# Kernel optimization log

Hardware: AMD Instinct MI355X
Metric: run time of the kernel (lower is better)

Reference implementation:

```python
import jax, jax.numpy as jnp
import numpy as np

N = 50000
E = 800000
F_IN = 64
F_OUT = 64


def setup_inputs() -> dict:
    key = jax.random.key(0)
    k1, k2, k3, k4, k5, k6 = jax.random.split(key, 6)
    x = jax.random.normal(k1, (N, F_IN), dtype=jnp.float32)
    x0 = jax.random.normal(k2, (N, F_IN), dtype=jnp.float32)
    edge_index = jax.random.randint(k3, (2, E), 0, N, dtype=jnp.int64)
    # Linear(in_channels, out_channels): weight [out, in], bias [out]
    bound = 1.0 / np.sqrt(F_IN)
    W_w = jax.random.uniform(k4, (F_OUT, F_IN), minval=-bound, maxval=bound, dtype=jnp.float32)
    W_b = jax.random.uniform(k5, (F_OUT,), minval=-bound, maxval=bound, dtype=jnp.float32)
    return {"x": x, "x0": x0, "edge_index": edge_index, "W_w": W_w, "W_b": W_b}


def reference(x, x0, edge_index, W_w, W_b):
    row, col = edge_index[0], edge_index[1]
    n = x.shape[0]
    # degree of each node as a destination (counts of col)
    d = jax.ops.segment_sum(jnp.ones_like(col, dtype=jnp.float32), col, num_segments=n)
    # per-edge symmetric normalization 1/sqrt(d[col]*d[row]); nan_to_num -> 0 where degree 0
    d_in = d[col]
    d_out = d[row]
    value = jnp.where((d_in > 0) & (d_out > 0),
                      jax.lax.rsqrt(jnp.maximum(d_in, 1.0)) * jax.lax.rsqrt(jnp.maximum(d_out, 1.0)),
                      0.0)
    # SpMM: adj has (row=col, col=row) so out[col_e] += value_e * x[row_e]
    msg = value[:, None] * x[row]                     # [E, F]
    agg = jax.ops.segment_sum(msg, col, num_segments=n)  # [N, F]
    # use_init=False, use_weight=True -> dense Linear
    return agg @ W_w.T + W_b
```

## Files before the change

### kernel.cpp

```cpp
#include <hip/hip_runtime.h>

#define NN 50000
#define NE 800000
#define FDIM 64
#define NB 8
#define P1B 768
#define RCAP 256
#define CAP 64
#define OVFCAP 16384
#define NPX 6250
#define GEMMB ((NN + 63) / 64)
#define E4 (NE / 4)
#define CHUNK4 ((E4 + P1B - 1) / P1B)

typedef float f32x4 __attribute__((ext_vector_type(4)));

__device__ __forceinline__ unsigned rne_bf16(float f) {
    unsigned u = __float_as_uint(f);
    return (u + 0x7fffu + ((u >> 16) & 1u)) >> 16;
}

__global__ __launch_bounds__(256) void k_part(
        const int4* __restrict__ row4, const int4* __restrict__ col4,
        unsigned* __restrict__ buckets, int* __restrict__ bcnt,
        int* __restrict__ cnt, unsigned* __restrict__ ovf, int* __restrict__ ovfcnt) {
    int gid = blockIdx.x * 256 + threadIdx.x;
    for (int i = gid; i < NN; i += P1B * 256) cnt[i] = 0;
    if (gid == 0) *ovfcnt = 0;

    __shared__ int lcnt[NB];
    if (threadIdx.x < NB) lcnt[threadIdx.x] = 0;
    __syncthreads();

    int start = blockIdx.x * CHUNK4;
    int end   = min(start + CHUNK4, E4);
    for (int i = start + (int)threadIdx.x; i < end; i += 256) {
        int4 r4 = row4[i];
        int4 c4 = col4[i];
        int rr[4] = {r4.x, r4.y, r4.z, r4.w};
        int cc[4] = {c4.x, c4.y, c4.z, c4.w};
#pragma unroll
        for (int t = 0; t < 4; ++t) {
            int c = cc[t];
            int b = (int)(((unsigned long long)(unsigned)c * 687195ull) >> 32);
            unsigned pk = ((unsigned)rr[t] << 16) | (unsigned)c;
            int slot = atomicAdd(&lcnt[b], 1);
            if (slot < RCAP)
                buckets[(size_t)(b * P1B + blockIdx.x) * RCAP + slot] = pk;
            else {
                int o = atomicAdd(ovfcnt, 1);
                if (o >= 0 && o < OVFCAP) ovf[o] = pk;
            }
        }
    }
    __syncthreads();
    if (threadIdx.x < NB)
        bcnt[threadIdx.x * P1B + blockIdx.x] = min(lcnt[threadIdx.x], RCAP);
}

__global__ __launch_bounds__(256) void k_gemm(const float* __restrict__ x,
                                              const float* __restrict__ W,
                                              unsigned* __restrict__ z) {
    __shared__ float Xl[64][68];
    __shared__ float Wt[64][68];

    for (int i = threadIdx.x; i < FDIM * FDIM; i += 256) {
        int o = i >> 6, k = i & 63;
        Wt[k][o] = W[i];
    }
    int tile = blockIdx.x * 64;
    for (int i = threadIdx.x; i < 64 * 16; i += 256) {
        int r = i >> 4, c4 = i & 15;
        int gr = tile + r;
        f32x4 v = (gr < NN) ? ((const f32x4*)x)[gr * 16 + c4]
                            : (f32x4){0.f, 0.f, 0.f, 0.f};
        *(f32x4*)&Xl[r][c4 * 4] = v;
    }
    __syncthreads();

    int tr = threadIdx.x >> 4;
    int tc = threadIdx.x & 15;

    float acc[4][4] = {};
#pragma unroll 1
    for (int k4 = 0; k4 < 16; ++k4) {
        f32x4 a[4], b[4];
#pragma unroll
        for (int i = 0; i < 4; ++i)
            a[i] = *(const f32x4*)&Xl[tr * 4 + i][k4 * 4];
#pragma unroll
        for (int kk = 0; kk < 4; ++kk)
            b[kk] = *(const f32x4*)&Wt[k4 * 4 + kk][tc * 4];
#pragma unroll
        for (int i = 0; i < 4; ++i) {
#pragma unroll
            for (int jj = 0; jj < 4; ++jj) {
                acc[i][jj] += a[i].x * b[0][jj] + a[i].y * b[1][jj]
                            + a[i].z * b[2][jj] + a[i].w * b[3][jj];
            }
        }
    }

#pragma unroll
    for (int i = 0; i < 4; ++i) {
        int gr = tile + tr * 4 + i;
        if (gr < NN) {
            unsigned u01 = rne_bf16(acc[i][0]) | (rne_bf16(acc[i][1]) << 16);
            unsigned u23 = rne_bf16(acc[i][2]) | (rne_bf16(acc[i][3]) << 16);
            ((uint2*)z)[gr * 16 + tc] = make_uint2(u01, u23);
        }
    }
}

__global__ __launch_bounds__(256) void k_fill(const unsigned* __restrict__ buckets,
                                              const int* __restrict__ bcnt,
                                              int* __restrict__ cnt,
                                              unsigned short* __restrict__ erow,
                                              unsigned* __restrict__ ovf,
                                              int* __restrict__ ovfcnt) {
    int k  = blockIdx.x & (NB - 1);
    int b1 = blockIdx.x >> 3;
    int m  = bcnt[k * P1B + b1];
    const unsigned* reg = buckets + (size_t)(k * P1B + b1) * RCAP;
    for (int i = threadIdx.x; i < m; i += 256) {
        unsigned pk = reg[i];
        int c = (int)(pk & 0xffffu), r = (int)(pk >> 16);
        int p = atomicAdd(&cnt[c], 1);
        if (p < CAP) erow[c * CAP + p] = (unsigned short)r;
        else {
            int o = atomicAdd(ovfcnt, 1);
            if (o >= 0 && o < OVFCAP) ovf[o] = pk;
        }
    }
}

__global__ __launch_bounds__(256) void k_gather(
        const int* __restrict__ cnt, const unsigned short* __restrict__ erow,
        const uint4* __restrict__ z4, const float* __restrict__ bias,
        const unsigned* __restrict__ ovf, const int* __restrict__ ovfcnt,
        float* __restrict__ out) {
    int lane = threadIdx.x & 63;
    int wv   = threadIdx.x >> 6;
    int xk   = blockIdx.x & 7;
    int sub  = blockIdx.x >> 3;
    int loc  = sub * 4 + wv;
    if (loc >= NPX) return;
    int node = xk * NPX + loc;

    int d  = cnt[node];
    int dc = min(d, CAP);
    int grp = lane >> 3, sl = lane & 7;
    int idx = (int)erow[node * CAP + lane];

    float a0=0,a1=0,a2=0,a3=0,a4=0,a5=0,a6=0,a7=0;
    int octets = (dc + 7) >> 3;
    for (int j = 0; j < octets; ++j) {
        int ei = j * 8 + grp;
        int rr = __shfl(idx, ei, 64);
        if (ei < dc) {
            int dr = cnt[rr];
            float sr = (dr > 0) ? rsqrtf((float)dr) : 0.f;
            uint4 u = z4[rr * 8 + sl];
            a0 += sr * __uint_as_float(u.x << 16);
            a1 += sr * __uint_as_float(u.x & 0xffff0000u);
            a2 += sr * __uint_as_float(u.y << 16);
            a3 += sr * __uint_as_float(u.y & 0xffff0000u);
            a4 += sr * __uint_as_float(u.z << 16);
            a5 += sr * __uint_as_float(u.z & 0xffff0000u);
            a6 += sr * __uint_as_float(u.w << 16);
            a7 += sr * __uint_as_float(u.w & 0xffff0000u);
        }
    }

    int ovn = min(*ovfcnt, OVFCAP);
    if (ovn > 0) {
        for (int i = 0; i < ovn; ++i) {
            unsigned pk = ovf[i];
            if ((int)(pk & 0xffffu) == node && grp == 0) {
                int rr = (int)(pk >> 16);
                int dr = cnt[rr];
                float sr = (dr > 0) ? rsqrtf((float)dr) : 0.f;
                uint4 u = z4[rr * 8 + sl];
                a0 += sr * __uint_as_float(u.x << 16);
                a1 += sr * __uint_as_float(u.x & 0xffff0000u);
                a2 += sr * __uint_as_float(u.y << 16);
                a3 += sr * __uint_as_float(u.y & 0xffff0000u);
                a4 += sr * __uint_as_float(u.z << 16);
                a5 += sr * __uint_as_float(u.z & 0xffff0000u);
                a6 += sr * __uint_as_float(u.w << 16);
                a7 += sr * __uint_as_float(u.w & 0xffff0000u);
            }
        }
    }

#pragma unroll
    for (int m = 8; m <= 32; m <<= 1) {
        a0 += __shfl_xor(a0, m, 64); a1 += __shfl_xor(a1, m, 64);
        a2 += __shfl_xor(a2, m, 64); a3 += __shfl_xor(a3, m, 64);
        a4 += __shfl_xor(a4, m, 64); a5 += __shfl_xor(a5, m, 64);
        a6 += __shfl_xor(a6, m, 64); a7 += __shfl_xor(a7, m, 64);
    }
    if (grp == 0) {
        float sc = (d > 0) ? rsqrtf((float)d) : 0.f;
        f32x4 b0 = ((const f32x4*)bias)[sl * 2];
        f32x4 b1 = ((const f32x4*)bias)[sl * 2 + 1];
        f32x4 o0 = {sc*a0+b0.x, sc*a1+b0.y, sc*a2+b0.z, sc*a3+b0.w};
        f32x4 o1 = {sc*a4+b1.x, sc*a5+b1.y, sc*a6+b1.z, sc*a7+b1.w};
        __builtin_nontemporal_store(o0, &((f32x4*)out)[node * 16 + sl * 2]);
        __builtin_nontemporal_store(o1, &((f32x4*)out)[node * 16 + sl * 2 + 1]);
    }
}

extern "C" void kernel_launch(void* const* d_in, const int* in_sizes, int n_in,
                              void* d_out, int out_size, void* d_ws, size_t ws_size,
                              hipStream_t stream) {
    const float* x   = (const float*)d_in[0];
    const int*   ei  = (const int*)d_in[2];
    const float* W_w = (const float*)d_in[3];
    const float* W_b = (const float*)d_in[4];
    float*       out = (float*)d_out;

    const int4* row4 = (const int4*)ei;
    const int4* col4 = (const int4*)(ei + NE);

    char* p = (char*)d_ws;
    auto alloc = [&](size_t bytes) {
        char* r = p;
        p += (bytes + 255) & ~(size_t)255;
        return r;
    };
    int*            cnt    = (int*)alloc(NN * sizeof(int));
    int*            ovfcnt = (int*)alloc(256);
    unsigned*       ovf    = (unsigned*)alloc(OVFCAP * sizeof(unsigned));
    int*            bcnt   = (int*)alloc(NB * P1B * sizeof(int));
    unsigned short* erow   = (unsigned short*)alloc((size_t)NN * CAP * sizeof(unsigned short));
    unsigned*       buckets = (unsigned*)alloc((size_t)NB * P1B * RCAP * sizeof(unsigned));
    unsigned*       z       = (unsigned*)alloc((size_t)NN * FDIM * 2);

    k_part  <<<P1B, 256, 0, stream>>>(row4, col4, buckets, bcnt, cnt, ovf, ovfcnt);
    k_gemm  <<<GEMMB, 256, 0, stream>>>(x, W_w, z);
    k_fill  <<<NB * P1B, 256, 0, stream>>>(buckets, bcnt, cnt, erow, ovf, ovfcnt);
    k_gather<<<NB * ((NPX + 3) / 4), 256, 0, stream>>>(cnt, erow, (const uint4*)z, W_b,
                                                       ovf, ovfcnt, out);
}
```

Before: 84.22 us.

## Fuse partition, GEMM, fill and gather into one cooperative persistent kernel

Replaces the four separate launches (edge partitioning, dense GEMM to bf16, CSR fill, gather) with a single cooperative kernel of 768 blocks. Work is grid-strided within each phase, and grid.sync() separates the fill and gather phases. This removes the launch gaps and idle time between kernel boundaries. The cost is a fixed, much smaller grid for the latency-bound gather phase, so fewer waves are in flight to hide random memory loads. The GEMM phase also adds extra block-level syncs, and each grid.sync carries its own overhead.

```diff
diff --git a/kernel.cpp b/kernel.cpp
--- a/kernel.cpp
+++ b/kernel.cpp
@@ -1,17 +1,20 @@
 #include <hip/hip_runtime.h>
+#include <hip/hip_cooperative_groups.h>
+
+namespace cg = cooperative_groups;
 
 #define NN 50000
 #define NE 800000
 #define FDIM 64
 #define NB 8
-#define P1B 768
+#define NBLK 768
 #define RCAP 256
 #define CAP 64
 #define OVFCAP 16384
 #define NPX 6250
 #define GEMMB ((NN + 63) / 64)
 #define E4 (NE / 4)
-#define CHUNK4 ((E4 + P1B - 1) / P1B)
+#define CHUNK4 ((E4 + NBLK - 1) / NBLK)
 
 typedef float f32x4 __attribute__((ext_vector_type(4)));
 
@@ -20,194 +23,202 @@
     return (u + 0x7fffu + ((u >> 16) & 1u)) >> 16;
 }
 
-__global__ __launch_bounds__(256) void k_part(
+__global__ __launch_bounds__(256) void k_all(
         const int4* __restrict__ row4, const int4* __restrict__ col4,
-        unsigned* __restrict__ buckets, int* __restrict__ bcnt,
-        int* __restrict__ cnt, unsigned* __restrict__ ovf, int* __restrict__ ovfcnt) {
-    int gid = blockIdx.x * 256 + threadIdx.x;
-    for (int i = gid; i < NN; i += P1B * 256) cnt[i] = 0;
-    if (gid == 0) *ovfcnt = 0;
-
-    __shared__ int lcnt[NB];
-    if (threadIdx.x < NB) lcnt[threadIdx.x] = 0;
-    __syncthreads();
-
-    int start = blockIdx.x * CHUNK4;
-    int end   = min(start + CHUNK4, E4);
-    for (int i = start + (int)threadIdx.x; i < end; i += 256) {
-        int4 r4 = row4[i];
-        int4 c4 = col4[i];
-        int rr[4] = {r4.x, r4.y, r4.z, r4.w};
-        int cc[4] = {c4.x, c4.y, c4.z, c4.w};
-#pragma unroll
-        for (int t = 0; t < 4; ++t) {
-            int c = cc[t];
-            int b = (int)(((unsigned long long)(unsigned)c * 687195ull) >> 32);
-            unsigned pk = ((unsigned)rr[t] << 16) | (unsigned)c;
-            int slot = atomicAdd(&lcnt[b], 1);
-            if (slot < RCAP)
-                buckets[(size_t)(b * P1B + blockIdx.x) * RCAP + slot] = pk;
-            else {
-                int o = atomicAdd(ovfcnt, 1);
-                if (o >= 0 && o < OVFCAP) ovf[o] = pk;
-            }
-        }
-    }
-    __syncthreads();
-    if (threadIdx.x < NB)
-        bcnt[threadIdx.x * P1B + blockIdx.x] = min(lcnt[threadIdx.x], RCAP);
-}
-
-__global__ __launch_bounds__(256) void k_gemm(const float* __restrict__ x,
-                                              const float* __restrict__ W,
-                                              unsigned* __restrict__ z) {
+        const float* __restrict__ x, const float* __restrict__ W,
+        const float* __restrict__ bias, float* __restrict__ out,
+        int* __restrict__ cnt, unsigned* __restrict__ ovf, int* __restrict__ ovfcnt,
+        int* __restrict__ bcnt, unsigned short* __restrict__ erow,
+        unsigned* __restrict__ buckets, unsigned* __restrict__ z) {
     __shared__ float Xl[64][68];
     __shared__ float Wt[64][68];
-
-    for (int i = threadIdx.x; i < FDIM * FDIM; i += 256) {
-        int o = i >> 6, k = i & 63;
-        Wt[k][o] = W[i];
-    }
-    int tile = blockIdx.x * 64;
-    for (int i = threadIdx.x; i < 64 * 16; i += 256) {
-        int r = i >> 4, c4 = i & 15;
-        int gr = tile + r;
-        f32x4 v = (gr < NN) ? ((const f32x4*)x)[gr * 16 + c4]
-                            : (f32x4){0.f, 0.f, 0.f, 0.f};
-        *(f32x4*)&Xl[r][c4 * 4] = v;
-    }
-    __syncthreads();
-
-    int tr = threadIdx.x >> 4;
-    int tc = threadIdx.x & 15;
-
-    float acc[4][4] = {};
-#pragma unroll 1
-    for (int k4 = 0; k4 < 16; ++k4) {
-        f32x4 a[4], b[4];
-#pragma unroll
-        for (int i = 0; i < 4; ++i)
-            a[i] = *(const f32x4*)&Xl[tr * 4 + i][k4 * 4];
-#pragma unroll
-        for (int kk = 0; kk < 4; ++kk)
-            b[kk] = *(const f32x4*)&Wt[k4 * 4 + kk][tc * 4];
-#pragma unroll
-        for (int i = 0; i < 4; ++i) {
-#pragma unroll
-            for (int jj = 0; jj < 4; ++jj) {
-                acc[i][jj] += a[i].x * b[0][jj] + a[i].y * b[1][jj]
-                            + a[i].z * b[2][jj] + a[i].w * b[3][jj];
-            }
-        }
-    }
-
-#pragma unroll
-    for (int i = 0; i < 4; ++i) {
-        int gr = tile + tr * 4 + i;
-        if (gr < NN) {
-            unsigned u01 = rne_bf16(acc[i][0]) | (rne_bf16(acc[i][1]) << 16);
-            unsigned u23 = rne_bf16(acc[i][2]) | (rne_bf16(acc[i][3]) << 16);
-            ((uint2*)z)[gr * 16 + tc] = make_uint2(u01, u23);
-        }
-    }
-}
-
-__global__ __launch_bounds__(256) void k_fill(const unsigned* __restrict__ buckets,
-                                              const int* __restrict__ bcnt,
-                                              int* __restrict__ cnt,
-                                              unsigned short* __restrict__ erow,
-                                              unsigned* __restrict__ ovf,
-                                              int* __restrict__ ovfcnt) {
-    int k  = blockIdx.x & (NB - 1);
-    int b1 = blockIdx.x >> 3;
-    int m  = bcnt[k * P1B + b1];
-    const unsigned* reg = buckets + (size_t)(k * P1B + b1) * RCAP;
-    for (int i = threadIdx.x; i < m; i += 256) {
-        unsigned pk = reg[i];
-        int c = (int)(pk & 0xffffu), r = (int)(pk >> 16);
-        int p = atomicAdd(&cnt[c], 1);
-        if (p < CAP) erow[c * CAP + p] = (unsigned short)r;
-        else {
-            int o = atomicAdd(ovfcnt, 1);
-            if (o >= 0 && o < OVFCAP) ovf[o] = pk;
-        }
-    }
-}
-
-__global__ __launch_bounds__(256) void k_gather(
-        const int* __restrict__ cnt, const unsigned short* __restrict__ erow,
-        const uint4* __restrict__ z4, const float* __restrict__ bias,
-        const unsigned* __restrict__ ovf, const int* __restrict__ ovfcnt,
-        float* __restrict__ out) {
-    int lane = threadIdx.x & 63;
-    int wv   = threadIdx.x >> 6;
-    int xk   = blockIdx.x & 7;
-    int sub  = blockIdx.x >> 3;
-    int loc  = sub * 4 + wv;
-    if (loc >= NPX) return;
-    int node = xk * NPX + loc;
-
-    int d  = cnt[node];
-    int dc = min(d, CAP);
-    int grp = lane >> 3, sl = lane & 7;
-    int idx = (int)erow[node * CAP + lane];
-
-    float a0=0,a1=0,a2=0,a3=0,a4=0,a5=0,a6=0,a7=0;
-    int octets = (dc + 7) >> 3;
-    for (int j = 0; j < octets; ++j) {
-        int ei = j * 8 + grp;
-        int rr = __shfl(idx, ei, 64);
-        if (ei < dc) {
-            int dr = cnt[rr];
-            float sr = (dr > 0) ? rsqrtf((float)dr) : 0.f;
-            uint4 u = z4[rr * 8 + sl];
-            a0 += sr * __uint_as_float(u.x << 16);
-            a1 += sr * __uint_as_float(u.x & 0xffff0000u);
-            a2 += sr * __uint_as_float(u.y << 16);
-            a3 += sr * __uint_as_float(u.y & 0xffff0000u);
-            a4 += sr * __uint_as_float(u.z << 16);
-            a5 += sr * __uint_as_float(u.z & 0xffff0000u);
-            a6 += sr * __uint_as_float(u.w << 16);
-            a7 += sr * __uint_as_float(u.w & 0xffff0000u);
-        }
-    }
-
-    int ovn = min(*ovfcnt, OVFCAP);
-    if (ovn > 0) {
-        for (int i = 0; i < ovn; ++i) {
-            unsigned pk = ovf[i];
-            if ((int)(pk & 0xffffu) == node && grp == 0) {
-                int rr = (int)(pk >> 16);
-                int dr = cnt[rr];
-                float sr = (dr > 0) ? rsqrtf((float)dr) : 0.f;
-                uint4 u = z4[rr * 8 + sl];
-                a0 += sr * __uint_as_float(u.x << 16);
-                a1 += sr * __uint_as_float(u.x & 0xffff0000u);
-                a2 += sr * __uint_as_float(u.y << 16);
-                a3 += sr * __uint_as_float(u.y & 0xffff0000u);
-                a4 += sr * __uint_as_float(u.z << 16);
-                a5 += sr * __uint_as_float(u.z & 0xffff0000u);
-                a6 += sr * __uint_as_float(u.w << 16);
-                a7 += sr * __uint_as_float(u.w & 0xffff0000u);
-            }
-        }
-    }
-
-#pragma unroll
-    for (int m = 8; m <= 32; m <<= 1) {
-        a0 += __shfl_xor(a0, m, 64); a1 += __shfl_xor(a1, m, 64);
-        a2 += __shfl_xor(a2, m, 64); a3 += __shfl_xor(a3, m, 64);
-        a4 += __shfl_xor(a4, m, 64); a5 += __shfl_xor(a5, m, 64);
-        a6 += __shfl_xor(a6, m, 64); a7 += __shfl_xor(a7, m, 64);
-    }
-    if (grp == 0) {
-        float sc = (d > 0) ? rsqrtf((float)d) : 0.f;
-        f32x4 b0 = ((const f32x4*)bias)[sl * 2];
-        f32x4 b1 = ((const f32x4*)bias)[sl * 2 + 1];
-        f32x4 o0 = {sc*a0+b0.x, sc*a1+b0.y, sc*a2+b0.z, sc*a3+b0.w};
-        f32x4 o1 = {sc*a4+b1.x, sc*a5+b1.y, sc*a6+b1.z, sc*a7+b1.w};
-        __builtin_nontemporal_store(o0, &((f32x4*)out)[node * 16 + sl * 2]);
-        __builtin_nontemporal_store(o1, &((f32x4*)out)[node * 16 + sl * 2 + 1]);
+    __shared__ int   lcnt[NB];
+
+    cg::grid_group grid = cg::this_grid();
+    int b   = blockIdx.x;
+    int tid = threadIdx.x;
+
+    {
+        int gid = b * 256 + tid;
+        for (int i = gid; i < NN; i += NBLK * 256) cnt[i] = 0;
+        if (gid == 0) *ovfcnt = 0;
+
+        if (tid < NB) lcnt[tid] = 0;
+        __syncthreads();
+
+        int start = b * CHUNK4;
+        int end   = min(start + CHUNK4, E4);
+        for (int i = start + tid; i < end; i += 256) {
+            int4 r4 = row4[i];
+            int4 c4 = col4[i];
+            int rr[4] = {r4.x, r4.y, r4.z, r4.w};
+            int cc[4] = {c4.x, c4.y, c4.z, c4.w};
+#pragma unroll
+            for (int t = 0; t < 4; ++t) {
+                int c = cc[t];
+                int bk = (int)(((unsigned long long)(unsigned)c * 687195ull) >> 32);
+                unsigned pk = ((unsigned)rr[t] << 16) | (unsigned)c;
+                int slot = atomicAdd(&lcnt[bk], 1);
+                if (slot < RCAP)
+                    buckets[(size_t)(bk * NBLK + b) * RCAP + slot] = pk;
+                else {
+                    int o = atomicAdd(ovfcnt, 1);
+                    if (o >= 0 && o < OVFCAP) ovf[o] = pk;
+                }
+            }
+        }
+        __syncthreads();
+        if (tid < NB)
+            bcnt[tid * NBLK + b] = min(lcnt[tid], RCAP);
+    }
+
+    {
+        for (int i = tid; i < FDIM * FDIM; i += 256) {
+            int o = i >> 6, k = i & 63;
+            Wt[k][o] = W[i];
+        }
+        int tr = tid >> 4;
+        int tc = tid & 15;
+#pragma unroll 1
+        for (int t = b; t < GEMMB; t += NBLK) {
+            __syncthreads();
+            int tile = t * 64;
+            for (int i = tid; i < 64 * 16; i += 256) {
+                int r = i >> 4, c4 = i & 15;
+                int gr = tile + r;
+                f32x4 v = (gr < NN) ? ((const f32x4*)x)[gr * 16 + c4]
+                                    : (f32x4){0.f, 0.f, 0.f, 0.f};
+                *(f32x4*)&Xl[r][c4 * 4] = v;
+            }
+            __syncthreads();
+
+            float acc[4][4] = {};
+#pragma unroll 1
+            for (int k4 = 0; k4 < 16; ++k4) {
+                f32x4 a[4], bb[4];
+#pragma unroll
+                for (int i = 0; i < 4; ++i)
+                    a[i] = *(const f32x4*)&Xl[tr * 4 + i][k4 * 4];
+#pragma unroll
+                for (int kk = 0; kk < 4; ++kk)
+                    bb[kk] = *(const f32x4*)&Wt[k4 * 4 + kk][tc * 4];
+#pragma unroll
+                for (int i = 0; i < 4; ++i) {
+#pragma unroll
+                    for (int jj = 0; jj < 4; ++jj) {
+                        acc[i][jj] += a[i].x * bb[0][jj] + a[i].y * bb[1][jj]
+                                    + a[i].z * bb[2][jj] + a[i].w * bb[3][jj];
+                    }
+                }
+            }
+#pragma unroll
+            for (int i = 0; i < 4; ++i) {
+                int gr = tile + tr * 4 + i;
+                if (gr < NN) {
+                    unsigned u01 = rne_bf16(acc[i][0]) | (rne_bf16(acc[i][1]) << 16);
+                    unsigned u23 = rne_bf16(acc[i][2]) | (rne_bf16(acc[i][3]) << 16);
+                    ((uint2*)z)[gr * 16 + tc] = make_uint2(u01, u23);
+                }
+            }
+        }
+    }
+
+    grid.sync();
+
+    {
+        int k = b & (NB - 1);
+#pragma unroll 1
+        for (int j = 0; j < 8; ++j) {
+            int b1 = (b >> 3) + (NBLK / NB) * j;
+            int m  = bcnt[k * NBLK + b1];
+            if (tid < m) {
+                unsigned pk = buckets[(size_t)(k * NBLK + b1) * RCAP + tid];
+                int c = (int)(pk & 0xffffu), r = (int)(pk >> 16);
+                int p = atomicAdd(&cnt[c], 1);
+                if (p < CAP) erow[c * CAP + p] = (unsigned short)r;
+                else {
+                    int o = atomicAdd(ovfcnt, 1);
+                    if (o >= 0 && o < OVFCAP) ovf[o] = pk;
+                }
+            }
+        }
+    }
+
+    grid.sync();
+
+    {
+        int lane = tid & 63;
+        int wv   = tid >> 6;
+        int xk   = b & 7;
+        int grp = lane >> 3, sl = lane & 7;
+        const uint4* z4 = (const uint4*)z;
+
+        int ovn = min(*ovfcnt, OVFCAP);
+
+#pragma unroll 1
+        for (int loc = (b >> 3) * 4 + wv; loc < NPX; loc += (NBLK / NB) * 4) {
+            int node = xk * NPX + loc;
+            int d  = cnt[node];
+            int dc = min(d, CAP);
+            int idx = (int)erow[node * CAP + lane];
+
+            float a0=0,a1=0,a2=0,a3=0,a4=0,a5=0,a6=0,a7=0;
+            int octets = (dc + 7) >> 3;
+            for (int j = 0; j < octets; ++j) {
+                int ei = j * 8 + grp;
+                int rr = __shfl(idx, ei, 64);
+                if (ei < dc) {
+                    int dr = cnt[rr];
+                    float sr = (dr > 0) ? rsqrtf((float)dr) : 0.f;
+                    uint4 u = z4[rr * 8 + sl];
+                    a0 += sr * __uint_as_float(u.x << 16);
+                    a1 += sr * __uint_as_float(u.x & 0xffff0000u);
+                    a2 += sr * __uint_as_float(u.y << 16);
+                    a3 += sr * __uint_as_float(u.y & 0xffff0000u);
+                    a4 += sr * __uint_as_float(u.z << 16);
+                    a5 += sr * __uint_as_float(u.z & 0xffff0000u);
+                    a6 += sr * __uint_as_float(u.w << 16);
+                    a7 += sr * __uint_as_float(u.w & 0xffff0000u);
+                }
+            }
+
+            if (ovn > 0) {
+                for (int i = 0; i < ovn; ++i) {
+                    unsigned pk = ovf[i];
+                    if ((int)(pk & 0xffffu) == node && grp == 0) {
+                        int rr = (int)(pk >> 16);
+                        int dr = cnt[rr];
+                        float sr = (dr > 0) ? rsqrtf((float)dr) : 0.f;
+                        uint4 u = z4[rr * 8 + sl];
+                        a0 += sr * __uint_as_float(u.x << 16);
+                        a1 += sr * __uint_as_float(u.x & 0xffff0000u);
+                        a2 += sr * __uint_as_float(u.y << 16);
+                        a3 += sr * __uint_as_float(u.y & 0xffff0000u);
+                        a4 += sr * __uint_as_float(u.z << 16);
+                        a5 += sr * __uint_as_float(u.z & 0xffff0000u);
+                        a6 += sr * __uint_as_float(u.w << 16);
+                        a7 += sr * __uint_as_float(u.w & 0xffff0000u);
+                    }
+                }
+            }
+
+#pragma unroll
+            for (int m = 8; m <= 32; m <<= 1) {
+                a0 += __shfl_xor(a0, m, 64); a1 += __shfl_xor(a1, m, 64);
+                a2 += __shfl_xor(a2, m, 64); a3 += __shfl_xor(a3, m, 64);
+                a4 += __shfl_xor(a4, m, 64); a5 += __shfl_xor(a5, m, 64);
+                a6 += __shfl_xor(a6, m, 64); a7 += __shfl_xor(a7, m, 64);
+            }
+            if (grp == 0) {
+                float sc = (d > 0) ? rsqrtf((float)d) : 0.f;
+                f32x4 b0 = ((const f32x4*)bias)[sl * 2];
+                f32x4 b1 = ((const f32x4*)bias)[sl * 2 + 1];
+                f32x4 o0 = {sc*a0+b0.x, sc*a1+b0.y, sc*a2+b0.z, sc*a3+b0.w};
+                f32x4 o1 = {sc*a4+b1.x, sc*a5+b1.y, sc*a6+b1.z, sc*a7+b1.w};
+                __builtin_nontemporal_store(o0, &((f32x4*)out)[node * 16 + sl * 2]);
+                __builtin_nontemporal_store(o1, &((f32x4*)out)[node * 16 + sl * 2 + 1]);
+            }
+        }
     }
 }
 
@@ -229,17 +240,17 @@
         p += (bytes + 255) & ~(size_t)255;
         return r;
     };
-    int*            cnt    = (int*)alloc(NN * sizeof(int));
-    int*            ovfcnt = (int*)alloc(256);
-    unsigned*       ovf    = (unsigned*)alloc(OVFCAP * sizeof(unsigned));
-    int*            bcnt   = (int*)alloc(NB * P1B * sizeof(int));
-    unsigned short* erow   = (unsigned short*)alloc((size_t)NN * CAP * sizeof(unsigned short));
-    unsigned*       buckets = (unsigned*)alloc((size_t)NB * P1B * RCAP * sizeof(unsigned));
+    int*            cnt     = (int*)alloc(NN * sizeof(int));
+    int*            ovfcnt  = (int*)alloc(256);
+    unsigned*       ovf     = (unsigned*)alloc(OVFCAP * sizeof(unsigned));
+    int*            bcnt    = (int*)alloc(NB * NBLK * sizeof(int));
+    unsigned short* erow    = (unsigned short*)alloc((size_t)NN * CAP * sizeof(unsigned short));
+    unsigned*       buckets = (unsigned*)alloc((size_t)NB * NBLK * RCAP * sizeof(unsigned));
     unsigned*       z       = (unsigned*)alloc((size_t)NN * FDIM * 2);
 
-    k_part  <<<P1B, 256, 0, stream>>>(row4, col4, buckets, bcnt, cnt, ovf, ovfcnt);
-    k_gemm  <<<GEMMB, 256, 0, stream>>>(x, W_w, z);
-    k_fill  <<<NB * P1B, 256, 0, stream>>>(buckets, bcnt, cnt, erow, ovf, ovfcnt);
-    k_gather<<<NB * ((NPX + 3) / 4), 256, 0, stream>>>(cnt, erow, (const uint4*)z, W_b,
-                                                       ovf, ovfcnt, out);
+    void* args[] = {(void*)&row4, (void*)&col4, (void*)&x, (void*)&W_w, (void*)&W_b,
+                    (void*)&out, (void*)&cnt, (void*)&ovf, (void*)&ovfcnt,
+                    (void*)&bcnt, (void*)&erow, (void*)&buckets, (void*)&z};
+    (void)hipLaunchCooperativeKernel((const void*)k_all, dim3(NBLK), dim3(256),
+                                     args, 0, stream);
 }
```

New measurement: 291.7 us. +246.3%, slower.
